# Performance work log

Measured on AMD Instinct MI355X. Metric: run time of the kernel, lower is better.

## Reference

```python
import jax, jax.numpy as jnp
import numpy as np

BN, N, FIN, FO, H = 4, 2048, 128, 64, 4
D = FO * H  # 256


def setup_inputs() -> dict:
    key = jax.random.key(0)
    ks = jax.random.split(key, 13)
    rnd = lambda k, s, sc=1.0: jax.random.normal(k, s, dtype=jnp.float32) * sc
    return {
        "x": rnd(ks[0], (BN, N, FIN)),
        "adj": rnd(ks[1], (BN, N, N)),
        "W_proj": rnd(ks[2], (D, FIN), 0.08),        # xavier-ish scale
        "score_src": rnd(ks[3], (H, FO), 0.1),        # (head_num, out_features)
        "score_tgt": rnd(ks[4], (H, FO), 0.1),
        "bias_out": jnp.zeros((D,), jnp.float32),
        "w_r": rnd(ks[5], (D, D), 0.06),
        "u_r": rnd(ks[6], (D, D), 0.06),
        "w_z": rnd(ks[7], (D, D), 0.06),
        "b_wz": jnp.full((D,), -2.0, jnp.float32),    # GRUGate init_bias
        "u_z": rnd(ks[8], (D, D), 0.06),
        "w_g": rnd(ks[9], (D, D), 0.06),
        "u_g": rnd(ks[10], (D, D), 0.06),
    }


def reference(x, adj, W_proj, score_src, score_tgt, bias_out,
              w_r, u_r, w_z, b_wz, u_z, w_g, u_g):
    bn, n = x.shape[:2]
    h, fo = score_src.shape
    # eval mode: dropout is identity
    proj_flat = x @ W_proj.T                                   # (bn, n, fo*h)
    # reshape splits last dim as (fo, h): head index fastest-varying
    proj = proj_flat.reshape(bn, n, fo, h).transpose(0, 3, 1, 2)  # (bn, h, n, fo)
    residual = proj_flat                                       # (bn, n, fo*h)
    s_src = jnp.einsum('bhnf,hf->bhn', proj, score_src)
    s_tgt = jnp.einsum('bhnf,hf->bhn', proj, score_tgt)
    scores = jax.nn.leaky_relu(s_src[..., :, None] + s_tgt[..., None, :], 0.2)
    scores = scores + adj[:, None]                             # (bn, h, n, n)
    attn = jax.nn.softmax(scores, axis=-1)
    out = jnp.einsum('bhij,bhjf->bhif', attn, proj)            # (bn, h, n, fo)
    out = out.transpose(0, 2, 1, 3).reshape(bn, n, h * fo)
    # GRUGate is computed in the torch source but its result is discarded
    z = jax.nn.sigmoid(out @ w_z.T + b_wz + residual @ u_z.T)
    r = jax.nn.sigmoid(out @ w_r.T + residual @ u_r.T)
    h_hat = jnp.tanh(out @ w_g.T + (r * residual) @ u_g.T)
    _gru = (1.0 - z) * residual + z * h_hat  # unused, matches source bug
    return jax.nn.elu(out + bias_out)
```

## Files before the change

### kernel.cpp

```cpp
#include <hip/hip_runtime.h>
#include <hip/hip_bf16.h>
#include <math.h>

#define BN_   4
#define NN_   2048
#define FIN_  128
#define FO_   64
#define H_    4
#define D_    256

typedef __attribute__((ext_vector_type(8))) short bf16x8;
typedef __attribute__((ext_vector_type(4))) float floatx4;

#define LOG2E 1.4426950408889634f

#if __has_builtin(__builtin_amdgcn_exp2f)
#define EXP2(x) __builtin_amdgcn_exp2f(x)
#else
#define EXP2(x) exp2f(x)
#endif

__device__ __forceinline__ float bf2f(short u) {
    union { unsigned int i; float f; } v;
    v.i = ((unsigned int)(unsigned short)u) << 16;
    return v.f;
}
__device__ __forceinline__ short f2bf(float f) {
    union { float f; unsigned int u; } v; v.f = f;
    unsigned int r = v.u + 0x7fffu + ((v.u >> 16) & 1u);
    return (short)(unsigned short)(r >> 16);
}

#if defined(__BF16_MANT_DIG__)
typedef __bf16 bfr2 __attribute__((ext_vector_type(2)));
__device__ __forceinline__ unsigned int pack_bf16(float a, float b) {
    union { bfr2 h; unsigned int u; } v;
    v.h = (bfr2){(__bf16)a, (__bf16)b};
    return v.u;
}
#else
__device__ __forceinline__ unsigned int pack_bf16(float a, float b) {
    return ((unsigned int)(unsigned short)f2bf(a)) |
           (((unsigned int)(unsigned short)f2bf(b)) << 16);
}
#endif

__device__ __forceinline__ bf16x8 load8f(const float* __restrict__ p) {
    floatx4 a = *(const floatx4*)p;
    floatx4 b = *(const floatx4*)(p + 4);
    union { bf16x8 v; unsigned int u[4]; } r;
    r.u[0] = pack_bf16(a[0], a[1]);
    r.u[1] = pack_bf16(a[2], a[3]);
    r.u[2] = pack_bf16(b[0], b[1]);
    r.u[3] = pack_bf16(b[2], b[3]);
    return r.v;
}

__global__ __launch_bounds__(256) void proj_kernel(
    const float* __restrict__ x,
    const float* __restrict__ wproj,
    const float* __restrict__ ssrc,
    const float* __restrict__ stgt,
    short* __restrict__ pt,
    float* __restrict__ sS,
    float* __restrict__ sT,
    int b0)
{
    const int tid  = threadIdx.x;
    const int wave = tid >> 6;
    const int lane = tid & 63;
    const int l16  = lane & 15;
    const int quad = lane >> 4;

    const int b_rel = blockIdx.z;
    const int b  = b0 + b_rel;
    const int h  = blockIdx.y;
    const int d0 = h * 64;
    const int j0 = blockIdx.x * 256 + wave * 64;

    floatx4 acc[4][4];
#pragma unroll
    for (int mi = 0; mi < 4; ++mi)
#pragma unroll
        for (int nj = 0; nj < 4; ++nj)
            acc[mi][nj] = (floatx4){0.f, 0.f, 0.f, 0.f};

#pragma unroll
    for (int kc = 0; kc < 4; ++kc) {
        const int c = kc * 32 + quad * 8;
        bf16x8 afr[4], bfr[4];
#pragma unroll
        for (int mi = 0; mi < 4; ++mi) {
            int f = (d0 + mi * 16 + l16) & 63;
            int srow = f * H_ + h;
            afr[mi] = load8f(wproj + srow * FIN_ + c);
        }
#pragma unroll
        for (int nj = 0; nj < 4; ++nj) {
            int j = j0 + nj * 16 + l16;
            bfr[nj] = load8f(x + ((size_t)b * NN_ + j) * FIN_ + c);
        }
#pragma unroll
        for (int mi = 0; mi < 4; ++mi)
#pragma unroll
            for (int nj = 0; nj < 4; ++nj)
                acc[mi][nj] = __builtin_amdgcn_mfma_f32_16x16x32_bf16(
                    afr[mi], bfr[nj], acc[mi][nj], 0, 0, 0);
    }

#pragma unroll
    for (int mi = 0; mi < 4; ++mi) {
#pragma unroll
        for (int r = 0; r < 4; ++r) {
            int dp = d0 + mi * 16 + quad * 4 + r;
            size_t base = ((size_t)b_rel * D_ + dp) * NN_;
#pragma unroll
            for (int nj = 0; nj < 4; ++nj) {
                int j = j0 + nj * 16 + l16;
                pt[base + j] = f2bf(acc[mi][nj][r]);
            }
        }
    }

    float wsv[4][4], wtv[4][4];
#pragma unroll
    for (int mi = 0; mi < 4; ++mi)
#pragma unroll
        for (int r = 0; r < 4; ++r) {
            int f = mi * 16 + quad * 4 + r;
            wsv[mi][r] = ssrc[h * FO_ + f];
            wtv[mi][r] = stgt[h * FO_ + f];
        }
    const size_t sbase = ((size_t)b_rel * H_ + h) * NN_;
#pragma unroll
    for (int nj = 0; nj < 4; ++nj) {
        float ps = 0.f, pg = 0.f;
#pragma unroll
        for (int mi = 0; mi < 4; ++mi)
#pragma unroll
            for (int r = 0; r < 4; ++r) {
                ps = fmaf(wsv[mi][r], acc[mi][nj][r], ps);
                pg = fmaf(wtv[mi][r], acc[mi][nj][r], pg);
            }
        ps += __shfl_xor(ps, 16, 64); ps += __shfl_xor(ps, 32, 64);
        pg += __shfl_xor(pg, 16, 64); pg += __shfl_xor(pg, 32, 64);
        if (quad == 0) {
            int j = j0 + nj * 16 + l16;
            sS[sbase + j] = ps;
            sT[sbase + j] = pg;
        }
    }
}

#define RSTRIDE 65
#define WSLOT   (RSTRIDE * 16 + 16)

__global__ __launch_bounds__(512, 2) void attn_kernel(
    const float* __restrict__ adj,
    const short* __restrict__ pt,
    const float* __restrict__ sS,
    const float* __restrict__ sT,
    const float* __restrict__ bias,
    float* __restrict__ out,
    int b0)
{
    __shared__ union {
        float st[8][4][256];
        float red[8][WSLOT];
    } sm;

    const int tid  = threadIdx.x;
    const int w    = tid >> 6;
    const int lane = tid & 63;
    const int l16  = lane & 15;
    const int quad = lane >> 4;

    const int b_rel = blockIdx.z;
    const int b  = b0 + b_rel;
    const int i0 = blockIdx.x * 16;

    const short* pt_b = pt + (size_t)b_rel * D_ * NN_;
    const size_t sb = (size_t)b_rel * H_ * NN_;

    {
        const int t = lane * 4;
#pragma unroll
        for (int h = 0; h < 4; ++h)
            *(floatx4*)&sm.st[w][h][t] =
                *(const floatx4*)&sT[sb + (size_t)h * NN_ + w * 256 + t];
    }

    float ssv[4];
#pragma unroll
    for (int h = 0; h < 4; ++h)
        ssv[h] = sS[sb + (size_t)h * NN_ + i0 + l16];

    const int qo = quad * 8;
    const float* adj_p = adj + ((size_t)b * NN_ + i0 + l16) * NN_ + w * 256 + qo;
    const short* ptr_hk[4][4];
#pragma unroll
    for (int h = 0; h < 4; ++h)
#pragma unroll
        for (int K = 0; K < 4; ++K)
            ptr_hk[h][K] = pt_b + (size_t)(h * FO_ + K * 16 + l16) * NN_ + w * 256 + qo;

    floatx4 acc[4][4];
#pragma unroll
    for (int h = 0; h < 4; ++h)
#pragma unroll
        for (int K = 0; K < 4; ++K)
            acc[h][K] = (floatx4){0.f, 0.f, 0.f, 0.f};
    float ls[4] = {0.f, 0.f, 0.f, 0.f};

#pragma unroll
    for (int jt = 0; jt < 8; ++jt) {
        const int o = jt * 32;
        floatx4 ajA = *(const floatx4*)(adj_p + o);
        floatx4 ajB = *(const floatx4*)(adj_p + o + 4);

#pragma unroll
        for (int h = 0; h < 4; ++h) {
            const float* stp = &sm.st[w][h][qo];
            floatx4 stA = *(const floatx4*)(stp + o);
            floatx4 stB = *(const floatx4*)(stp + o + 4);
            bf16x8 bfr[4];
#pragma unroll
            for (int K = 0; K < 4; ++K)
                bfr[K] = *(const bf16x8*)(ptr_hk[h][K] + o);

            auto sc = [&](float stv, float av) {
                float s = ssv[h] + stv;
                s = fmaxf(s, 0.2f * s);
                return EXP2((s + av) * LOG2E);
            };
            float w0 = sc(stA[0], ajA[0]), w1 = sc(stA[1], ajA[1]);
            float w2 = sc(stA[2], ajA[2]), w3 = sc(stA[3], ajA[3]);
            float w4 = sc(stB[0], ajB[0]), w5 = sc(stB[1], ajB[1]);
            float w6 = sc(stB[2], ajB[2]), w7 = sc(stB[3], ajB[7 - 7 + 3]);
            ls[h] += ((w0 + w1) + (w2 + w3)) + ((w4 + w5) + (w6 + w7));
            union { bf16x8 v; unsigned int u[4]; } a0;
            a0.u[0] = pack_bf16(w0, w1);
            a0.u[1] = pack_bf16(w2, w3);
            a0.u[2] = pack_bf16(w4, w5);
            a0.u[3] = pack_bf16(w6, w7);
#pragma unroll
            for (int K = 0; K < 4; ++K)
                acc[h][K] = __builtin_amdgcn_mfma_f32_16x16x32_bf16(
                    a0.v, bfr[K], acc[h][K], 0, 0, 0);
        }
    }

#pragma unroll
    for (int h = 0; h < 4; ++h) {
        ls[h] += __shfl_xor(ls[h], 16, 64);
        ls[h] += __shfl_xor(ls[h], 32, 64);
    }

#pragma unroll
    for (int h = 0; h < 4; ++h) {
        __syncthreads();
#pragma unroll
        for (int K = 0; K < 4; ++K)
#pragma unroll
            for (int r = 0; r < 4; ++r)
                sm.red[w][(quad * 4 + r) * RSTRIDE + K * 16 + l16] = acc[h][K][r];
        if (quad == 0)
            sm.red[w][16 * RSTRIDE + l16] = ls[h];
        __syncthreads();
#pragma unroll
        for (int p = 0; p < 2; ++p) {
            int e   = tid + p * 512;
            int row = e >> 6;
            int col = e & 63;
            float s = 0.f, l = 0.f;
#pragma unroll
            for (int ww = 0; ww < 8; ++ww) {
                s += sm.red[ww][row * RSTRIDE + col];
                l += sm.red[ww][16 * RSTRIDE + row];
            }
            float v = s / l + bias[h * FO_ + col];
            v = (v > 0.f) ? v : expm1f(v);
            out[((size_t)b * NN_ + i0 + row) * D_ + h * FO_ + col] = v;
        }
    }
}

extern "C" void kernel_launch(void* const* d_in, const int* in_sizes, int n_in,
                              void* d_out, int out_size, void* d_ws, size_t ws_size,
                              hipStream_t stream) {
    const float* x     = (const float*)d_in[0];
    const float* adj   = (const float*)d_in[1];
    const float* wproj = (const float*)d_in[2];
    const float* ssrc  = (const float*)d_in[3];
    const float* stgt  = (const float*)d_in[4];
    const float* bias  = (const float*)d_in[5];
    float* out = (float*)d_out;

    const size_t SLAB  = (size_t)D_ * NN_ * 2;
    const size_t SSLAB = (size_t)2 * H_ * NN_ * 4;
    int nb = (int)(ws_size / (SLAB + SSLAB));
    if (nb < 1) nb = 1;
    if (nb > 4) nb = 4;

    short* pt = (short*)d_ws;
    float* sv = (float*)((char*)d_ws + (size_t)nb * SLAB);
    float* sS = sv;
    float* sT = sv + (size_t)nb * H_ * NN_;

    for (int bb0 = 0; bb0 < BN_; bb0 += nb) {
        int cnt = (BN_ - bb0 < nb) ? (BN_ - bb0) : nb;
        proj_kernel<<<dim3(NN_ / 256, H_, cnt), 256, 0, stream>>>(
            x, wproj, ssrc, stgt, pt, sS, sT, bb0);
        attn_kernel<<<dim3(NN_ / 16, 1, cnt), 512, 0, stream>>>(
            adj, pt, sS, sT, bias, out, bb0);
    }
}
```

Measured before the change: 193.5 us.

## Split attention heads across two grid blocks to raise parallelism

The attention kernel now handles two heads per block instead of four and adds a grid y-dimension over head pairs, doubling the block count. Registers and LDS per block drop (accumulators halve), which may improve occupancy and wave scheduling. The cost is that each adj row tile is now read twice, once per head-pair block, which adds HBM traffic for the largest input.

```diff
diff --git a/kernel.cpp b/kernel.cpp
--- a/kernel.cpp
+++ b/kernel.cpp
@@ -54,6 +54,12 @@
     r.u[2] = pack_bf16(b[0], b[1]);
     r.u[3] = pack_bf16(b[2], b[3]);
     return r.v;
+}
+
+__device__ __forceinline__ float score_exp(float ssv, float stv, float av) {
+    float s = ssv + stv;
+    s = fmaxf(s, 0.2f * s);
+    return EXP2((s + av) * LOG2E);
 }
 
 __global__ __launch_bounds__(256) void proj_kernel(
@@ -165,7 +171,7 @@
     int b0)
 {
     __shared__ union {
-        float st[8][4][256];
+        float st[8][2][256];
         float red[8][WSLOT];
     } sm;
 
@@ -177,6 +183,7 @@
 
     const int b_rel = blockIdx.z;
     const int b  = b0 + b_rel;
+    const int hp = blockIdx.y;
     const int i0 = blockIdx.x * 16;
 
     const short* pt_b = pt + (size_t)b_rel * D_ * NN_;
@@ -185,32 +192,33 @@
     {
         const int t = lane * 4;
 #pragma unroll
-        for (int h = 0; h < 4; ++h)
-            *(floatx4*)&sm.st[w][h][t] =
-                *(const floatx4*)&sT[sb + (size_t)h * NN_ + w * 256 + t];
-    }
-
-    float ssv[4];
-#pragma unroll
-    for (int h = 0; h < 4; ++h)
-        ssv[h] = sS[sb + (size_t)h * NN_ + i0 + l16];
+        for (int u = 0; u < 2; ++u)
+            *(floatx4*)&sm.st[w][u][t] =
+                *(const floatx4*)&sT[sb + (size_t)(hp * 2 + u) * NN_ + w * 256 + t];
+    }
+
+    float ssv[2];
+#pragma unroll
+    for (int u = 0; u < 2; ++u)
+        ssv[u] = sS[sb + (size_t)(hp * 2 + u) * NN_ + i0 + l16];
 
     const int qo = quad * 8;
     const float* adj_p = adj + ((size_t)b * NN_ + i0 + l16) * NN_ + w * 256 + qo;
-    const short* ptr_hk[4][4];
-#pragma unroll
-    for (int h = 0; h < 4; ++h)
+    const short* ptr_hk[2][4];
+#pragma unroll
+    for (int u = 0; u < 2; ++u)
 #pragma unroll
         for (int K = 0; K < 4; ++K)
-            ptr_hk[h][K] = pt_b + (size_t)(h * FO_ + K * 16 + l16) * NN_ + w * 256 + qo;
-
-    floatx4 acc[4][4];
-#pragma unroll
-    for (int h = 0; h < 4; ++h)
+            ptr_hk[u][K] = pt_b + (size_t)((hp * 2 + u) * FO_ + K * 16 + l16) * NN_
+                         + w * 256 + qo;
+
+    floatx4 acc[2][4];
+#pragma unroll
+    for (int u = 0; u < 2; ++u)
 #pragma unroll
         for (int K = 0; K < 4; ++K)
-            acc[h][K] = (floatx4){0.f, 0.f, 0.f, 0.f};
-    float ls[4] = {0.f, 0.f, 0.f, 0.f};
+            acc[u][K] = (floatx4){0.f, 0.f, 0.f, 0.f};
+    float ls[2] = {0.f, 0.f};
 
 #pragma unroll
     for (int jt = 0; jt < 8; ++jt) {
@@ -219,54 +227,54 @@
         floatx4 ajB = *(const floatx4*)(adj_p + o + 4);
 
 #pragma unroll
-        for (int h = 0; h < 4; ++h) {
-            const float* stp = &sm.st[w][h][qo];
+        for (int u = 0; u < 2; ++u) {
+            const float* stp = &sm.st[w][u][qo];
             floatx4 stA = *(const floatx4*)(stp + o);
             floatx4 stB = *(const floatx4*)(stp + o + 4);
             bf16x8 bfr[4];
 #pragma unroll
             for (int K = 0; K < 4; ++K)
-                bfr[K] = *(const bf16x8*)(ptr_hk[h][K] + o);
-
-            auto sc = [&](float stv, float av) {
-                float s = ssv[h] + stv;
-                s = fmaxf(s, 0.2f * s);
-                return EXP2((s + av) * LOG2E);
-            };
-            float w0 = sc(stA[0], ajA[0]), w1 = sc(stA[1], ajA[1]);
-            float w2 = sc(stA[2], ajA[2]), w3 = sc(stA[3], ajA[3]);
-            float w4 = sc(stB[0], ajB[0]), w5 = sc(stB[1], ajB[1]);
-            float w6 = sc(stB[2], ajB[2]), w7 = sc(stB[3], ajB[7 - 7 + 3]);
-            ls[h] += ((w0 + w1) + (w2 + w3)) + ((w4 + w5) + (w6 + w7));
-            union { bf16x8 v; unsigned int u[4]; } a0;
-            a0.u[0] = pack_bf16(w0, w1);
-            a0.u[1] = pack_bf16(w2, w3);
-            a0.u[2] = pack_bf16(w4, w5);
-            a0.u[3] = pack_bf16(w6, w7);
+                bfr[K] = *(const bf16x8*)(ptr_hk[u][K] + o);
+
+            float w0 = score_exp(ssv[u], stA[0], ajA[0]);
+            float w1 = score_exp(ssv[u], stA[1], ajA[1]);
+            float w2 = score_exp(ssv[u], stA[2], ajA[2]);
+            float w3 = score_exp(ssv[u], stA[3], ajA[3]);
+            float w4 = score_exp(ssv[u], stB[0], ajB[0]);
+            float w5 = score_exp(ssv[u], stB[1], ajB[1]);
+            float w6 = score_exp(ssv[u], stB[2], ajB[2]);
+            float w7 = score_exp(ssv[u], stB[3], ajB[3]);
+            ls[u] += ((w0 + w1) + (w2 + w3)) + ((w4 + w5) + (w6 + w7));
+            union { bf16x8 v; unsigned int u4[4]; } a0;
+            a0.u4[0] = pack_bf16(w0, w1);
+            a0.u4[1] = pack_bf16(w2, w3);
+            a0.u4[2] = pack_bf16(w4, w5);
+            a0.u4[3] = pack_bf16(w6, w7);
 #pragma unroll
             for (int K = 0; K < 4; ++K)
-                acc[h][K] = __builtin_amdgcn_mfma_f32_16x16x32_bf16(
-                    a0.v, bfr[K], acc[h][K], 0, 0, 0);
-        }
-    }
-
-#pragma unroll
-    for (int h = 0; h < 4; ++h) {
-        ls[h] += __shfl_xor(ls[h], 16, 64);
-        ls[h] += __shfl_xor(ls[h], 32, 64);
-    }
-
-#pragma unroll
-    for (int h = 0; h < 4; ++h) {
+                acc[u][K] = __builtin_amdgcn_mfma_f32_16x16x32_bf16(
+                    a0.v, bfr[K], acc[u][K], 0, 0, 0);
+        }
+    }
+
+#pragma unroll
+    for (int u = 0; u < 2; ++u) {
+        ls[u] += __shfl_xor(ls[u], 16, 64);
+        ls[u] += __shfl_xor(ls[u], 32, 64);
+    }
+
+#pragma unroll
+    for (int u = 0; u < 2; ++u) {
         __syncthreads();
 #pragma unroll
         for (int K = 0; K < 4; ++K)
 #pragma unroll
             for (int r = 0; r < 4; ++r)
-                sm.red[w][(quad * 4 + r) * RSTRIDE + K * 16 + l16] = acc[h][K][r];
+                sm.red[w][(quad * 4 + r) * RSTRIDE + K * 16 + l16] = acc[u][K][r];
         if (quad == 0)
-            sm.red[w][16 * RSTRIDE + l16] = ls[h];
+            sm.red[w][16 * RSTRIDE + l16] = ls[u];
         __syncthreads();
+        const int hh = hp * 2 + u;
 #pragma unroll
         for (int p = 0; p < 2; ++p) {
             int e   = tid + p * 512;
@@ -278,9 +286,9 @@
                 s += sm.red[ww][row * RSTRIDE + col];
                 l += sm.red[ww][16 * RSTRIDE + row];
             }
-            float v = s / l + bias[h * FO_ + col];
+            float v = s / l + bias[hh * FO_ + col];
             v = (v > 0.f) ? v : expm1f(v);
-            out[((size_t)b * NN_ + i0 + row) * D_ + h * FO_ + col] = v;
+            out[((size_t)b * NN_ + i0 + row) * D_ + hh * FO_ + col] = v;
         }
     }
 }
@@ -311,7 +319,7 @@
         int cnt = (BN_ - bb0 < nb) ? (BN_ - bb0) : nb;
         proj_kernel<<<dim3(NN_ / 256, H_, cnt), 256, 0, stream>>>(
             x, wproj, ssrc, stgt, pt, sS, sT, bb0);
-        attn_kernel<<<dim3(NN_ / 16, 1, cnt), 512, 0, stream>>>(
+        attn_kernel<<<dim3(NN_ / 16, H_ / 2, cnt), 512, 0, stream>>>(
             adj, pt, sS, sT, bias, out, bb0);
     }
 }
```

Result: slower. 200.4 us (+3.5%).

## Tile projected features into MFMA-fragment layout and stage adj through LDS

Applied to the files above, without the earlier changes.

The projection kernel now writes the bf16 projected features in a tiled layout, so each MFMA B fragment is one contiguous 16-byte-per-lane chunk rather than 16 strided row reads. The attention kernel stages adjacency rows through a per-wave LDS buffer using row-coalesced loads, and prefetches the next 32-column tile into registers while the current tile is computed. This is meant to improve global memory coalescing for both adj and the feature operand. The cost is extra LDS traffic and more registers. No barrier is placed between the LDS write and read of the staged tile, so correctness relies on wave-synchronous execution within each wave's private slot.

```diff
diff --git a/kernel.cpp b/kernel.cpp
--- a/kernel.cpp
+++ b/kernel.cpp
@@ -54,6 +54,12 @@
     r.u[2] = pack_bf16(b[0], b[1]);
     r.u[3] = pack_bf16(b[2], b[3]);
     return r.v;
+}
+
+__device__ __forceinline__ float score_exp(float ssv, float stv, float av) {
+    float s = ssv + stv;
+    s = fmaxf(s, 0.2f * s);
+    return EXP2((s + av) * LOG2E);
 }
 
 __global__ __launch_bounds__(256) void proj_kernel(
@@ -108,16 +114,19 @@
                     afr[mi], bfr[nj], acc[mi][nj], 0, 0, 0);
     }
 
+    const size_t hbase = ((size_t)b_rel * H_ + h) * (size_t)(64 * 2048);
+    const int jt0 = j0 >> 5;
 #pragma unroll
     for (int mi = 0; mi < 4; ++mi) {
 #pragma unroll
         for (int r = 0; r < 4; ++r) {
-            int dp = d0 + mi * 16 + quad * 4 + r;
-            size_t base = ((size_t)b_rel * D_ + dp) * NN_;
+            const int f15 = quad * 4 + r;
 #pragma unroll
             for (int nj = 0; nj < 4; ++nj) {
-                int j = j0 + nj * 16 + l16;
-                pt[base + j] = f2bf(acc[mi][nj][r]);
+                const int tile = jt0 + (nj >> 1);
+                const int jsub = (nj & 1) * 2 + (l16 >> 3);
+                pt[hbase + (size_t)tile * 2048 + mi * 512 + jsub * 128
+                   + f15 * 8 + (l16 & 7)] = f2bf(acc[mi][nj][r]);
             }
         }
     }
@@ -165,7 +174,10 @@
     int b0)
 {
     __shared__ union {
-        float st[8][4][256];
+        struct {
+            float adjs[8][16][36];
+            float st[8][4][256];
+        } m;
         float red[8][WSLOT];
     } sm;
 
@@ -174,19 +186,21 @@
     const int lane = tid & 63;
     const int l16  = lane & 15;
     const int quad = lane >> 4;
+    const int r8   = lane >> 3;
+    const int c4   = (lane & 7) * 4;
 
     const int b_rel = blockIdx.z;
     const int b  = b0 + b_rel;
     const int i0 = blockIdx.x * 16;
 
-    const short* pt_b = pt + (size_t)b_rel * D_ * NN_;
+    const short* pt2_b = pt + (size_t)b_rel * H_ * (size_t)(64 * 2048);
     const size_t sb = (size_t)b_rel * H_ * NN_;
 
     {
         const int t = lane * 4;
 #pragma unroll
         for (int h = 0; h < 4; ++h)
-            *(floatx4*)&sm.st[w][h][t] =
+            *(floatx4*)&sm.m.st[w][h][t] =
                 *(const floatx4*)&sT[sb + (size_t)h * NN_ + w * 256 + t];
     }
 
@@ -195,14 +209,7 @@
     for (int h = 0; h < 4; ++h)
         ssv[h] = sS[sb + (size_t)h * NN_ + i0 + l16];
 
-    const int qo = quad * 8;
-    const float* adj_p = adj + ((size_t)b * NN_ + i0 + l16) * NN_ + w * 256 + qo;
-    const short* ptr_hk[4][4];
-#pragma unroll
-    for (int h = 0; h < 4; ++h)
-#pragma unroll
-        for (int K = 0; K < 4; ++K)
-            ptr_hk[h][K] = pt_b + (size_t)(h * FO_ + K * 16 + l16) * NN_ + w * 256 + qo;
+    const float* adj_base = adj + ((size_t)b * NN_ + i0) * NN_ + w * 256;
 
     floatx4 acc[4][4];
 #pragma unroll
@@ -212,41 +219,61 @@
             acc[h][K] = (floatx4){0.f, 0.f, 0.f, 0.f};
     float ls[4] = {0.f, 0.f, 0.f, 0.f};
 
+    floatx4 areg0 = *(const floatx4*)(adj_base + (size_t)r8 * NN_ + c4);
+    floatx4 areg1 = *(const floatx4*)(adj_base + (size_t)(8 + r8) * NN_ + c4);
+    *(floatx4*)&sm.m.adjs[w][r8][c4]     = areg0;
+    *(floatx4*)&sm.m.adjs[w][8 + r8][c4] = areg1;
+
+    const int lo8 = lane * 8;
+
 #pragma unroll
     for (int jt = 0; jt < 8; ++jt) {
-        const int o = jt * 32;
-        floatx4 ajA = *(const floatx4*)(adj_p + o);
-        floatx4 ajB = *(const floatx4*)(adj_p + o + 4);
-
-#pragma unroll
-        for (int h = 0; h < 4; ++h) {
-            const float* stp = &sm.st[w][h][qo];
+        const int o  = jt * 32;
+        const int qo = quad * 8;
+
+        if (jt < 7) {
+            areg0 = *(const floatx4*)(adj_base + (size_t)r8 * NN_ + o + 32 + c4);
+            areg1 = *(const floatx4*)(adj_base + (size_t)(8 + r8) * NN_ + o + 32 + c4);
+        }
+
+        floatx4 ajA = *(const floatx4*)&sm.m.adjs[w][l16][qo];
+        floatx4 ajB = *(const floatx4*)&sm.m.adjs[w][l16][qo + 4];
+
+#pragma unroll
+        for (int u = 0; u < 4; ++u) {
+            const short* fb = pt2_b + ((size_t)u * 64 + (w * 8 + jt)) * 2048 + lo8;
+            bf16x8 bfr[4];
+#pragma unroll
+            for (int K = 0; K < 4; ++K)
+                bfr[K] = *(const bf16x8*)(fb + K * 512);
+
+            const float* stp = &sm.m.st[w][u][qo];
             floatx4 stA = *(const floatx4*)(stp + o);
             floatx4 stB = *(const floatx4*)(stp + o + 4);
-            bf16x8 bfr[4];
+
+            float w0 = score_exp(ssv[u], stA[0], ajA[0]);
+            float w1 = score_exp(ssv[u], stA[1], ajA[1]);
+            float w2 = score_exp(ssv[u], stA[2], ajA[2]);
+            float w3 = score_exp(ssv[u], stA[3], ajA[3]);
+            float w4 = score_exp(ssv[u], stB[0], ajB[0]);
+            float w5 = score_exp(ssv[u], stB[1], ajB[1]);
+            float w6 = score_exp(ssv[u], stB[2], ajB[2]);
+            float w7 = score_exp(ssv[u], stB[3], ajB[3]);
+            ls[u] += ((w0 + w1) + (w2 + w3)) + ((w4 + w5) + (w6 + w7));
+            union { bf16x8 v; unsigned int u4[4]; } a0;
+            a0.u4[0] = pack_bf16(w0, w1);
+            a0.u4[1] = pack_bf16(w2, w3);
+            a0.u4[2] = pack_bf16(w4, w5);
+            a0.u4[3] = pack_bf16(w6, w7);
 #pragma unroll
             for (int K = 0; K < 4; ++K)
-                bfr[K] = *(const bf16x8*)(ptr_hk[h][K] + o);
-
-            auto sc = [&](float stv, float av) {
-                float s = ssv[h] + stv;
-                s = fmaxf(s, 0.2f * s);
-                return EXP2((s + av) * LOG2E);
-            };
-            float w0 = sc(stA[0], ajA[0]), w1 = sc(stA[1], ajA[1]);
-            float w2 = sc(stA[2], ajA[2]), w3 = sc(stA[3], ajA[3]);
-            float w4 = sc(stB[0], ajB[0]), w5 = sc(stB[1], ajB[1]);
-            float w6 = sc(stB[2], ajB[2]), w7 = sc(stB[3], ajB[7 - 7 + 3]);
-            ls[h] += ((w0 + w1) + (w2 + w3)) + ((w4 + w5) + (w6 + w7));
-            union { bf16x8 v; unsigned int u[4]; } a0;
-            a0.u[0] = pack_bf16(w0, w1);
-            a0.u[1] = pack_bf16(w2, w3);
-            a0.u[2] = pack_bf16(w4, w5);
-            a0.u[3] = pack_bf16(w6, w7);
-#pragma unroll
-            for (int K = 0; K < 4; ++K)
-                acc[h][K] = __builtin_amdgcn_mfma_f32_16x16x32_bf16(
-                    a0.v, bfr[K], acc[h][K], 0, 0, 0);
+                acc[u][K] = __builtin_amdgcn_mfma_f32_16x16x32_bf16(
+                    a0.v, bfr[K], acc[u][K], 0, 0, 0);
+        }
+
+        if (jt < 7) {
+            *(floatx4*)&sm.m.adjs[w][r8][c4]     = areg0;
+            *(floatx4*)&sm.m.adjs[w][8 + r8][c4] = areg1;
         }
     }
 
```

After: 164.1 us. -15.2%, faster.
